# Kernel optimization log

Measured on AMD Instinct MI355X. Metric: run time of the kernel, lower is better.

## Reference

```python
import jax, jax.numpy as jnp
import numpy as np

B = 128            # trees per batch
D = 6              # complete binary tree depth
NPT = 2 ** (D + 1) - 1   # 127 nodes per tree
H = 450            # JTNN hidden size
V = 780            # junction-tree vocab size


def _build_forest():
    # complete binary trees; node 0 of each tree is the root
    child = np.arange(1, NPT)
    parent = (child - 1) // 2
    offs = (np.arange(B) * NPT)[:, None]
    ch = (child[None, :] + offs).ravel()
    pa = (parent[None, :] + offs).ravel()
    Eup = B * (NPT - 1)
    E = 2 * Eup
    # up (child->parent) edges first, then down (parent->child); +1 dummy pad row
    src = np.concatenate([ch, pa, [0]]).astype(np.int32)
    dst = np.concatenate([pa, ch, [0]]).astype(np.int32)
    rev = np.concatenate([np.arange(Eup) + Eup, np.arange(Eup), [E]]).astype(np.int32)
    depth_child = np.floor(np.log2(child + 1)).astype(np.int64)  # 1..D
    toff = np.arange(B)[:, None] * (NPT - 1)
    rows = []
    for d in range(D, 0, -1):        # bottom-up: deepest child level first
        t = np.nonzero(depth_child == d)[0]
        rows.append((t[None, :] + toff).ravel())
    for d in range(1, D + 1):        # top-down
        t = np.nonzero(depth_child == d)[0]
        rows.append((t[None, :] + toff).ravel() + Eup)
    Lmax = max(len(r) for r in rows)
    sched = np.full((len(rows), Lmax), E, dtype=np.int32)   # pad with dummy id E
    for i, r in enumerate(rows):
        sched[i, :len(r)] = r
    return src, dst, rev, sched


def setup_inputs() -> dict:
    key = jax.random.key(0)
    ks = jax.random.split(key, 8)
    src, dst, rev, sched = _build_forest()
    n_nodes = B * NPT
    p = lambda k, shp: jax.random.normal(k, shp, jnp.float32) * 0.05
    return {
        'wid': jax.random.randint(ks[0], (n_nodes,), 0, V).astype(jnp.int32),
        'src': jnp.asarray(src), 'dst': jnp.asarray(dst), 'rev': jnp.asarray(rev),
        'sched': jnp.asarray(sched),
        'emb': p(ks[1], (V, H)),
        'Wz': p(ks[2], (2 * H, H)), 'bz': jnp.zeros((H,), jnp.float32),
        'Wr': p(ks[3], (H, H)),
        'Ur': p(ks[4], (H, H)), 'bur': jnp.zeros((H,), jnp.float32),
        'Wh': p(ks[5], (2 * H, H)), 'bh': jnp.zeros((H,), jnp.float32),
        'Wg': p(ks[6], (2 * H, H)), 'bg': jnp.zeros((H,), jnp.float32),
    }


def _forward(wid, src, dst, rev, sched, emb, Wz, bz, Wr, Ur, bur, Wh, bh, Wg, bg):
    n_nodes = wid.shape[0]
    E = src.shape[0] - 1              # last slot is a dummy pad row
    x = emb[wid]                      # [N, H] node embeddings
    m = jnp.zeros((E + 1, x.shape[1]), x.dtype)   # edge messages (line-graph node state)
    rm = jnp.zeros_like(m)
    dstE = dst[:E]
    for lvl in range(sched.shape[0]):             # static number of tree levels
        eid = sched[lvl]                          # [Lmax], padded with E
        # pull: s/accum_rm = sum over predecessor line-graph nodes, i.e.
        # sum of m over in-edges of src[e] minus the backtracking (reverse) edge
        node_m = jax.ops.segment_sum(m[:E], dstE, num_segments=n_nodes)
        node_rm = jax.ops.segment_sum(rm[:E], dstE, num_segments=n_nodes)
        se, de = src[eid], dst[eid]
        s = node_m[se] - m[rev[eid]]
        arm = node_rm[se] - rm[rev[eid]]
        sx, dx = x[se], x[de]
        # GRUUpdate (DGL JTNN)
        z = jax.nn.sigmoid(jnp.concatenate([sx, s], 1) @ Wz + bz)
        mt = jnp.tanh(jnp.concatenate([sx, arm], 1) @ Wh + bh)
        m_new = (1.0 - z) * s + z * mt
        r = jax.nn.sigmoid(dx @ Wr + m_new @ Ur + bur)   # W_r has no bias
        m = m.at[eid].set(m_new)
        rm = rm.at[eid].set(r * m_new)
    # update_all: gather messages into destination nodes, then EncoderGatherUpdate
    node_m = jax.ops.segment_sum(m[:E], dstE, num_segments=n_nodes)
    h = jax.nn.relu(jnp.concatenate([x, node_m], 1) @ Wg + bg)   # [N, H]
    return h


def reference(wid, src, dst, rev, sched, emb, Wz, bz, Wr, Ur, bur, Wh, bh, Wg, bg):
    # returns h for all nodes; root_vecs = h[node_offsets] (roots are every NPT-th node)
    return _forward(wid, src, dst, rev, sched, emb, Wz, bz, Wr, Ur, bur, Wh, bh, Wg, bg)
```

## Files before the change

kernel.cpp:

```cpp
#include <hip/hip_runtime.h>
#include <math.h>

#define NTREES 128
#define NPT 127
#define NNODES (NTREES*NPT)
#define EUP (NTREES*(NPT-1))
#define HDIM 450
#define HP 512
#define LMAX 8192
#define NLVL 12

typedef unsigned short u16;
typedef __attribute__((ext_vector_type(8))) short bf16x8;
typedef __attribute__((ext_vector_type(4))) float f32x4;

__device__ __forceinline__ float sigmoidf_(float x) { return 1.f / (1.f + expf(-x)); }
__device__ __forceinline__ u16 f2b(float x) {
  unsigned u = __float_as_uint(x);
  return (u16)((u + 0x7FFFu + ((u >> 16) & 1u)) >> 16);
}
__device__ __forceinline__ float b2f(u16 h) { return __uint_as_float(((unsigned)h) << 16); }
__device__ __forceinline__ bf16x8 sub8(bf16x8 a, bf16x8 b) {
  bf16x8 r;
#pragma unroll
  for (int i = 0; i < 8; ++i) r[i] = (short)f2b(b2f((u16)a[i]) - b2f((u16)b[i]));
  return r;
}

__device__ __forceinline__ u16* ldsp(u16* base, int row, int slot) {
  return base + row * 64 + ((slot ^ (row & 7)) << 3);
}
#define MFMA(a, b, c) __builtin_amdgcn_mfma_f32_16x16x32_bf16(a, b, c, 0, 0, 0)

__global__ void zero_ws(float4* __restrict__ p, int n4) {
  int i = blockIdx.x * 256 + threadIdx.x;
  int stride = gridDim.x * 256;
  for (; i < n4; i += stride) p[i] = make_float4(0.f, 0.f, 0.f, 0.f);
}

__global__ void prep_pad(const float* __restrict__ Wz, const float* __restrict__ Wh,
                         const float* __restrict__ Wr, const float* __restrict__ Ur,
                         const float* __restrict__ Wg,
                         const float* __restrict__ bz, const float* __restrict__ bh,
                         const float* __restrict__ bur, const float* __restrict__ bg,
                         u16* __restrict__ WpreT, u16* __restrict__ WzbT,
                         u16* __restrict__ WhbT, u16* __restrict__ UrT,
                         u16* __restrict__ WgT, float* __restrict__ biasp) {
  int idx = blockIdx.x * 256 + threadIdx.x;
  if (idx < 1536 * 512) {
    int n = idx >> 9, k = idx & 511;
    int sel = n >> 9, j = n & 511;
    float v = 0.f;
    if (k < HDIM && j < HDIM) {
// ... 43 lines not shown
  int row = gid >> 6, g = gid & 63;
  int j0 = g * 8;
  const float* er = emb + (size_t)wid[row] * HDIM;
  float f[8] = {0.f, 0.f, 0.f, 0.f, 0.f, 0.f, 0.f, 0.f};
  if (j0 <= 440) {
#pragma unroll
    for (int q = 0; q < 4; ++q) {
      float2 p = *(const float2*)(er + j0 + q * 2);
      f[q * 2] = p.x; f[q * 2 + 1] = p.y;
    }
  } else if (j0 == 448) {
    f[0] = er[448]; f[1] = er[449];
  }
  bf16x8 v;
#pragma unroll
  for (int q = 0; q < 8; ++q) v[q] = (short)f2b(f[q]);
  *(bf16x8*)(xp + (size_t)row * HP + j0) = v;
}

__global__ __launch_bounds__(256, 4) void mfma_pre(
    const u16* __restrict__ xp, const u16* __restrict__ WpreT,
    u16* __restrict__ Xzh, u16* __restrict__ Xr) {
  __shared__ u16 Al[64 * 64], Bl[64 * 64];
  int tid = threadIdx.x;
  int n0 = blockIdx.x * 64, m0 = blockIdx.y * 64;
  int l = tid & 63, w = tid >> 6, wr = w >> 1, wc = w & 1, lr = l & 15, lq = l >> 4;
  int sr = tid >> 2, skc = tid & 3;
  const u16* abase = xp + (size_t)(m0 + sr) * HP + skc * 16;
  const u16* bbase = WpreT + (size_t)(n0 + sr) * HP + skc * 16;
  f32x4 acc[2][2] = {};
  for (int kt = 0; kt < HP; kt += 64) {
    *(bf16x8*)ldsp(Al, sr, 2 * skc) = ((const bf16x8*)(abase + kt))[0];
    *(bf16x8*)ldsp(Al, sr, 2 * skc + 1) = ((const bf16x8*)(abase + kt))[1];
    *(bf16x8*)ldsp(Bl, sr, 2 * skc) = ((const bf16x8*)(bbase + kt))[0];
    *(bf16x8*)ldsp(Bl, sr, 2 * skc + 1) = ((const bf16x8*)(bbase + kt))[1];
    __syncthreads();
#pragma unroll
    for (int kk = 0; kk < 64; kk += 32) {
      int slot = (kk >> 3) + lq;
      bf16x8 fa0 = *(bf16x8*)ldsp(Al, wr * 32 + lr, slot);
      bf16x8 fa1 = *(bf16x8*)ldsp(Al, wr * 32 + 16 + lr, slot);
      bf16x8 fb0 = *(bf16x8*)ldsp(Bl, wc * 32 + lr, slot);
      bf16x8 fb1 = *(bf16x8*)ldsp(Bl, wc * 32 + 16 + lr, slot);
      acc[0][0] = MFMA(fa0, fb0, acc[0][0]); acc[0][1] = MFMA(fa0, fb1, acc[0][1]);
      acc[1][0] = MFMA(fa1, fb0, acc[1][0]); acc[1][1] = MFMA(fa1, fb1, acc[1][1]);
    }
    __syncthreads();
  }
#pragma unroll
  for (int fi = 0; fi < 2; ++fi)
#pragma unroll
    for (int fj = 0; fj < 2; ++fj) {
      int colg = n0 + wc * 32 + fj * 16 + lr;
#pragma unroll
      for (int reg = 0; reg < 4; ++reg) {
        int row = m0 + wr * 32 + fi * 16 + lq * 4 + reg;
        u16 o = f2b(acc[fi][fj][reg]);
        if (colg < 1024) Xzh[(size_t)row * 1024 + colg] = o;
        else Xr[(size_t)row * HP + (colg - 1024)] = o;
      }
    }
}

__global__ void leaf_lvl0(const int* __restrict__ sched0, const int* __restrict__ src,
                          const u16* __restrict__ Xzh, const float* __restrict__ biasp,
                          u16* __restrict__ mup) {
  int gid = blockIdx.x * 256 + threadIdx.x;
  int r = gid >> 7, g = gid & 127;
  int e = sched0[r];
  int se = src[e];
  int col = g * 4;
  ushort4 xz = *(const ushort4*)(Xzh + (size_t)se * 1024 + col);
  ushort4 xh = *(const ushort4*)(Xzh + (size_t)se * 1024 + 512 + col);
  float4 bz = *(const float4*)(biasp + col);
  float4 bh = *(const float4*)(biasp + 512 + col);
  ushort4 o;
  o.x = f2b(sigmoidf_(b2f(xz.x) + bz.x) * tanhf(b2f(xh.x) + bh.x));
  o.y = f2b(sigmoidf_(b2f(xz.y) + bz.y) * tanhf(b2f(xh.y) + bh.y));
  o.z = f2b(sigmoidf_(b2f(xz.z) + bz.z) * tanhf(b2f(xh.z) + bh.z));
  o.w = f2b(sigmoidf_(b2f(xz.w) + bz.w) * tanhf(b2f(xh.w) + bh.w));
  *(ushort4*)(mup + (size_t)e * HP + col) = o;
}

__global__ __launch_bounds__(256, 4) void mfma_lvl1_up(
    const int* __restrict__ schedrow, const int* __restrict__ src,
    const u16* __restrict__ node_m, const u16* __restrict__ node_rm,
    const u16* __restrict__ Xzh, const u16* __restrict__ WzbT,
    const u16* __restrict__ WhbT, const float* __restrict__ biasp,
    u16* __restrict__ mup) {
  __shared__ u16 Asl[64 * 64], Aal[64 * 64], Bzl[64 * 64], Btl[64 * 64];
  __shared__ int e_s[64], se_s[64];
  int tid = threadIdx.x;
  int n0 = blockIdx.x * 64, m0 = blockIdx.y * 64;
  if (tid < 64) { int e = schedrow[m0 + tid]; e_s[tid] = e; se_s[tid] = src[e]; }
  __syncthreads();
  int l = tid & 63, w = tid >> 6, wr = w >> 1, wc = w & 1, lr = l & 15, lq = l >> 4;
  int sr = tid >> 2, skc = tid & 3;
  int se_st = se_s[sr];
  const u16* pmb = node_m + (size_t)se_st * HP + skc * 16;
  const u16* prb = node_rm + (size_t)se_st * HP + skc * 16;
  const u16* bzb = WzbT + (size_t)(n0 + sr) * HP + skc * 16;
  const u16* btb = WhbT + (size_t)(n0 + sr) * HP + skc * 16;
  f32x4 accZ[2][2] = {}, accT[2][2] = {};
  for (int kt = 0; kt < HP; kt += 64) {
    *(bf16x8*)ldsp(Asl, sr, 2 * skc) = ((const bf16x8*)(pmb + kt))[0];
    *(bf16x8*)ldsp(Asl, sr, 2 * skc + 1) = ((const bf16x8*)(pmb + kt))[1];
    *(bf16x8*)ldsp(Aal, sr, 2 * skc) = ((const bf16x8*)(prb + kt))[0];
    *(bf16x8*)ldsp(Aal, sr, 2 * skc + 1) = ((const bf16x8*)(prb + kt))[1];
    *(bf16x8*)ldsp(Bzl, sr, 2 * skc) = ((const bf16x8*)(bzb + kt))[0];
    *(bf16x8*)ldsp(Bzl, sr, 2 * skc + 1) = ((const bf16x8*)(bzb + kt))[1];
    *(bf16x8*)ldsp(Btl, sr, 2 * skc) = ((const bf16x8*)(btb + kt))[0];
    *(bf16x8*)ldsp(Btl, sr, 2 * skc + 1) = ((const bf16x8*)(btb + kt))[1];
    __syncthreads();
#pragma unroll
    for (int kk = 0; kk < 64; kk += 32) {
      int slot = (kk >> 3) + lq;
      bf16x8 a0 = *(bf16x8*)ldsp(Asl, wr * 32 + lr, slot);
      bf16x8 a1 = *(bf16x8*)ldsp(Asl, wr * 32 + 16 + lr, slot);
      bf16x8 c0 = *(bf16x8*)ldsp(Aal, wr * 32 + lr, slot);
      bf16x8 c1 = *(bf16x8*)ldsp(Aal, wr * 32 + 16 + lr, slot);
      bf16x8 z0 = *(bf16x8*)ldsp(Bzl, wc * 32 + lr, slot);
      bf16x8 z1 = *(bf16x8*)ldsp(Bzl, wc * 32 + 16 + lr, slot);
      bf16x8 t0 = *(bf16x8*)ldsp(Btl, wc * 32 + lr, slot);
      bf16x8 t1 = *(bf16x8*)ldsp(Btl, wc * 32 + 16 + lr, slot);
      accZ[0][0] = MFMA(a0, z0, accZ[0][0]); accZ[0][1] = MFMA(a0, z1, accZ[0][1]);
      accZ[1][0] = MFMA(a1, z0, accZ[1][0]); accZ[1][1] = MFMA(a1, z1, accZ[1][1]);
      accT[0][0] = MFMA(c0, t0, accT[0][0]); accT[0][1] = MFMA(c0, t1, accT[0][1]);
      accT[1][0] = MFMA(c1, t0, accT[1][0]); accT[1][1] = MFMA(c1, t1, accT[1][1]);
    }
    __syncthreads();
  }
#pragma unroll
  for (int fi = 0; fi < 2; ++fi)
#pragma unroll
    for (int fj = 0; fj < 2; ++fj) {
      int colg = n0 + wc * 32 + fj * 16 + lr;
#pragma unroll
      for (int reg = 0; reg < 4; ++reg) {
        int row = wr * 32 + fi * 16 + lq * 4 + reg;
        int e = e_s[row], se = se_s[row];
        float xz = b2f(Xzh[(size_t)se * 1024 + colg]);
        float xh = b2f(Xzh[(size_t)se * 1024 + 512 + colg]);
        float sv = b2f(node_m[(size_t)se * HP + colg]);
        float z = sigmoidf_(accZ[fi][fj][reg] + xz + biasp[colg]);
        float t = tanhf(accT[fi][fj][reg] + xh + biasp[512 + colg]);
        mup[(size_t)e * HP + colg] = f2b((1.f - z) * sv + z * t);
      }
    }
}

__global__ __launch_bounds__(256, 4) void mfma_lvl1_down(
    const int* __restrict__ schedrow, const int* __restrict__ src,
    const u16* __restrict__ node_m, const u16* __restrict__ node_rm,
    const u16* __restrict__ mup, const u16* __restrict__ rmup,
    const u16* __restrict__ Xzh, const u16* __restrict__ WzbT,
    const u16* __restrict__ WhbT, const float* __restrict__ biasp,
    u16* __restrict__ dtmp) {
  __shared__ u16 Asl[64 * 64], Aal[64 * 64], Bzl[64 * 64], Btl[64 * 64];
  __shared__ int se_s[64], eu_s[64];
  int tid = threadIdx.x;
  int n0 = blockIdx.x * 64, m0 = blockIdx.y * 64;
  if (tid < 64) { int e = schedrow[m0 + tid]; eu_s[tid] = e - EUP; se_s[tid] = src[e]; }
  __syncthreads();
  int l = tid & 63, w = tid >> 6, wr = w >> 1, wc = w & 1, lr = l & 15, lq = l >> 4;
  int sr = tid >> 2, skc = tid & 3;
  int se_st = se_s[sr], eu_st = eu_s[sr];
  const u16* pmb = node_m + (size_t)se_st * HP + skc * 16;
  const u16* pub = mup + (size_t)eu_st * HP + skc * 16;
  const u16* prb = node_rm + (size_t)se_st * HP + skc * 16;
  const u16* pvb = rmup + (size_t)eu_st * HP + skc * 16;
  const u16* bzb = WzbT + (size_t)(n0 + sr) * HP + skc * 16;
  const u16* btb = WhbT + (size_t)(n0 + sr) * HP + skc * 16;
  f32x4 accZ[2][2] = {}, accT[2][2] = {};
  for (int kt = 0; kt < HP; kt += 64) {
    *(bf16x8*)ldsp(Asl, sr, 2 * skc) = sub8(((const bf16x8*)(pmb + kt))[0], ((const bf16x8*)(pub + kt))[0]);
    *(bf16x8*)ldsp(Asl, sr, 2 * skc + 1) = sub8(((const bf16x8*)(pmb + kt))[1], ((const bf16x8*)(pub + kt))[1]);
    *(bf16x8*)ldsp(Aal, sr, 2 * skc) = sub8(((const bf16x8*)(prb + kt))[0], ((const bf16x8*)(pvb + kt))[0]);
    *(bf16x8*)ldsp(Aal, sr, 2 * skc + 1) = sub8(((const bf16x8*)(prb + kt))[1], ((const bf16x8*)(pvb + kt))[1]);
    *(bf16x8*)ldsp(Bzl, sr, 2 * skc) = ((const bf16x8*)(bzb + kt))[0];
    *(bf16x8*)ldsp(Bzl, sr, 2 * skc + 1) = ((const bf16x8*)(bzb + kt))[1];
    *(bf16x8*)ldsp(Btl, sr, 2 * skc) = ((const bf16x8*)(btb + kt))[0];
    *(bf16x8*)ldsp(Btl, sr, 2 * skc + 1) = ((const bf16x8*)(btb + kt))[1];
    __syncthreads();
#pragma unroll
    for (int kk = 0; kk < 64; kk += 32) {
      int slot = (kk >> 3) + lq;
      bf16x8 a0 = *(bf16x8*)ldsp(Asl, wr * 32 + lr, slot);
      bf16x8 a1 = *(bf16x8*)ldsp(Asl, wr * 32 + 16 + lr, slot);
      bf16x8 c0 = *(bf16x8*)ldsp(Aal, wr * 32 + lr, slot);
      bf16x8 c1 = *(bf16x8*)ldsp(Aal, wr * 32 + 16 + lr, slot);
      bf16x8 z0 = *(bf16x8*)ldsp(Bzl, wc * 32 + lr, slot);
      bf16x8 z1 = *(bf16x8*)ldsp(Bzl, wc * 32 + 16 + lr, slot);
      bf16x8 t0 = *(bf16x8*)ldsp(Btl, wc * 32 + lr, slot);
      bf16x8 t1 = *(bf16x8*)ldsp(Btl, wc * 32 + 16 + lr, slot);
      accZ[0][0] = MFMA(a0, z0, accZ[0][0]); accZ[0][1] = MFMA(a0, z1, accZ[0][1]);
      accZ[1][0] = MFMA(a1, z0, accZ[1][0]); accZ[1][1] = MFMA(a1, z1, accZ[1][1]);
      accT[0][0] = MFMA(c0, t0, accT[0][0]); accT[0][1] = MFMA(c0, t1, accT[0][1]);
      accT[1][0] = MFMA(c1, t0, accT[1][0]); accT[1][1] = MFMA(c1, t1, accT[1][1]);
    }
    __syncthreads();
  }
#pragma unroll
  for (int fi = 0; fi < 2; ++fi)
#pragma unroll
    for (int fj = 0; fj < 2; ++fj) {
      int colg = n0 + wc * 32 + fj * 16 + lr;
#pragma unroll
      for (int reg = 0; reg < 4; ++reg) {
        int row = wr * 32 + fi * 16 + lq * 4 + reg;
        int se = se_s[row], eu = eu_s[row];
        float xz = b2f(Xzh[(size_t)se * 1024 + colg]);
        float xh = b2f(Xzh[(size_t)se * 1024 + 512 + colg]);
        float sv = b2f(node_m[(size_t)se * HP + colg]) - b2f(mup[(size_t)eu * HP + colg]);
        float z = sigmoidf_(accZ[fi][fj][reg] + xz + biasp[colg]);
        float t = tanhf(accT[fi][fj][reg] + xh + biasp[512 + colg]);
        dtmp[(size_t)(m0 + row) * HP + colg] = f2b((1.f - z) * sv + z * t);
      }
    }
}

__global__ __launch_bounds__(256, 4) void mfma_lvl2_up(
    const int* __restrict__ schedrow, const int* __restrict__ dst,
    const u16* __restrict__ mup, u16* __restrict__ rmup,
    u16* __restrict__ node_m, u16* __restrict__ node_rm,
    const u16* __restrict__ Xr, const u16* __restrict__ UrT,
    const float* __restrict__ biasp) {
  __shared__ u16 Al[64 * 64], Bl[64 * 64];
  __shared__ int e_s[64], de_s[64];
  int tid = threadIdx.x;
  int n0 = blockIdx.x * 64, m0 = blockIdx.y * 64;
  if (tid < 64) { int e = schedrow[m0 + tid]; e_s[tid] = e; de_s[tid] = dst[e]; }
  __syncthreads();
  int l = tid & 63, w = tid >> 6, wr = w >> 1, wc = w & 1, lr = l & 15, lq = l >> 4;
  int sr = tid >> 2, skc = tid & 3;
  const u16* ab = mup + (size_t)e_s[sr] * HP + skc * 16;
  const u16* bb = UrT + (size_t)(n0 + sr) * HP + skc * 16;
  f32x4 acc[2][2] = {};
  for (int kt = 0; kt < HP; kt += 64) {
    *(bf16x8*)ldsp(Al, sr, 2 * skc) = ((const bf16x8*)(ab + kt))[0];
    *(bf16x8*)ldsp(Al, sr, 2 * skc + 1) = ((const bf16x8*)(ab + kt))[1];
    *(bf16x8*)ldsp(Bl, sr, 2 * skc) = ((const bf16x8*)(bb + kt))[0];
    *(bf16x8*)ldsp(Bl, sr, 2 * skc + 1) = ((const bf16x8*)(bb + kt))[1];
    __syncthreads();
#pragma unroll
    for (int kk = 0; kk < 64; kk += 32) {
      int slot = (kk >> 3) + lq;
      bf16x8 fa0 = *(bf16x8*)ldsp(Al, wr * 32 + lr, slot);
      bf16x8 fa1 = *(bf16x8*)ldsp(Al, wr * 32 + 16 + lr, slot);
      bf16x8 fb0 = *(bf16x8*)ldsp(Bl, wc * 32 + lr, slot);
      bf16x8 fb1 = *(bf16x8*)ldsp(Bl, wc * 32 + 16 + lr, slot);
      acc[0][0] = MFMA(fa0, fb0, acc[0][0]); acc[0][1] = MFMA(fa0, fb1, acc[0][1]);
      acc[1][0] = MFMA(fa1, fb0, acc[1][0]); acc[1][1] = MFMA(fa1, fb1, acc[1][1]);
    }
    __syncthreads();
  }
#pragma unroll
  for (int fi = 0; fi < 2; ++fi)
#pragma unroll
    for (int fj = 0; fj < 2; ++fj) {
      int colg = n0 + wc * 32 + fj * 16 + lr;
      int rowbase = wr * 32 + fi * 16 + lq * 4;
      float mv[4], rmv[4];
#pragma unroll
      for (int reg = 0; reg < 4; ++reg) {
        int row = rowbase + reg;
        int e = e_s[row], de = de_s[row];
        mv[reg] = b2f(mup[(size_t)e * HP + colg]);
        float r = sigmoidf_(acc[fi][fj][reg] + b2f(Xr[(size_t)de * HP + colg]) + biasp[1024 + colg]);
        rmv[reg] = r * mv[reg];
        rmup[(size_t)e * HP + colg] = f2b(rmv[reg]);
      }
      int de0 = de_s[rowbase], de2 = de_s[rowbase + 2];
      node_m[(size_t)de0 * HP + colg] = f2b(mv[0] + mv[1]);
      node_rm[(size_t)de0 * HP + colg] = f2b(rmv[0] + rmv[1]);
      node_m[(size_t)de2 * HP + colg] = f2b(mv[2] + mv[3]);
      node_rm[(size_t)de2 * HP + colg] = f2b(rmv[2] + rmv[3]);
    }
}

__global__ __launch_bounds__(256, 4) void mfma_lvl2_down(
    const int* __restrict__ schedrow, const int* __restrict__ dst,
    const u16* __restrict__ dtmp,
    u16* __restrict__ node_m, u16* __restrict__ node_rm,
    const u16* __restrict__ Xr, const u16* __restrict__ UrT,
    const float* __restrict__ biasp) {
  __shared__ u16 Al[64 * 64], Bl[64 * 64];
  __shared__ int de_s[64];
  int tid = threadIdx.x;
  int n0 = blockIdx.x * 64, m0 = blockIdx.y * 64;
  if (tid < 64) de_s[tid] = dst[schedrow[m0 + tid]];
  __syncthreads();
  int l = tid & 63, w = tid >> 6, wr = w >> 1, wc = w & 1, lr = l & 15, lq = l >> 4;
  int sr = tid >> 2, skc = tid & 3;
  const u16* ab = dtmp + (size_t)(m0 + sr) * HP + skc * 16;
  const u16* bb = UrT + (size_t)(n0 + sr) * HP + skc * 16;
  f32x4 acc[2][2] = {};
  for (int kt = 0; kt < HP; kt += 64) {
    *(bf16x8*)ldsp(Al, sr, 2 * skc) = ((const bf16x8*)(ab + kt))[0];
    *(bf16x8*)ldsp(Al, sr, 2 * skc + 1) = ((const bf16x8*)(ab + kt))[1];
    *(bf16x8*)ldsp(Bl, sr, 2 * skc) = ((const bf16x8*)(bb + kt))[0];
    *(bf16x8*)ldsp(Bl, sr, 2 * skc + 1) = ((const bf16x8*)(bb + kt))[1];
    __syncthreads();
#pragma unroll
    for (int kk = 0; kk < 64; kk += 32) {
      int slot = (kk >> 3) + lq;
      bf16x8 fa0 = *(bf16x8*)ldsp(Al, wr * 32 + lr, slot);
      bf16x8 fa1 = *(bf16x8*)ldsp(Al, wr * 32 + 16 + lr, slot);
      bf16x8 fb0 = *(bf16x8*)ldsp(Bl, wc * 32 + lr, slot);
      bf16x8 fb1 = *(bf16x8*)ldsp(Bl, wc * 32 + 16 + lr, slot);
      acc[0][0] = MFMA(fa0, fb0, acc[0][0]); acc[0][1] = MFMA(fa0, fb1, acc[0][1]);
      acc[1][0] = MFMA(fa1, fb0, acc[1][0]); acc[1][1] = MFMA(fa1, fb1, acc[1][1]);
    }
    __syncthreads();
  }
#pragma unroll
  for (int fi = 0; fi < 2; ++fi)
#pragma unroll
    for (int fj = 0; fj < 2; ++fj) {
      int colg = n0 + wc * 32 + fj * 16 + lr;
#pragma unroll
      for (int reg = 0; reg < 4; ++reg) {
        int row = wr * 32 + fi * 16 + lq * 4 + reg;
        int de = de_s[row];
        size_t nidx = (size_t)de * HP + colg;
        float mv = b2f(dtmp[(size_t)(m0 + row) * HP + colg]);
        float r = sigmoidf_(acc[fi][fj][reg] + b2f(Xr[nidx]) + biasp[1024 + colg]);
        node_m[nidx] = f2b(b2f(node_m[nidx]) + mv);
        node_rm[nidx] = f2b(b2f(node_rm[nidx]) + r * mv);
      }
    }
}

__global__ __launch_bounds__(256, 4) void mfma_final(
    const u16* __restrict__ xp, const u16* __restrict__ node_m,
    const u16* __restrict__ WgT, const float* __restrict__ biasp,
    float* __restrict__ out) {
  __shared__ u16 Al[64 * 64], Bl[64 * 64];
  int tid = threadIdx.x;
  int n0 = blockIdx.x * 64, m0 = blockIdx.y * 64;
  int l = tid & 63, w = tid >> 6, wr = w >> 1, wc = w & 1, lr = l & 15, lq = l >> 4;
  int sr = tid >> 2, skc = tid & 3;
  const u16* axb = xp + (size_t)(m0 + sr) * HP + skc * 16;
  const u16* anb = node_m + (size_t)(m0 + sr) * HP + skc * 16;
  const u16* bb = WgT + (size_t)(n0 + sr) * 1024 + skc * 16;
  f32x4 acc[2][2] = {};
  for (int kt = 0; kt < 1024; kt += 64) {
    const u16* ap = (kt < HP) ? (axb + kt) : (anb + (kt - HP));
    *(bf16x8*)ldsp(Al, sr, 2 * skc) = ((const bf16x8*)ap)[0];
    *(bf16x8*)ldsp(Al, sr, 2 * skc + 1) = ((const bf16x8*)ap)[1];
    *(bf16x8*)ldsp(Bl, sr, 2 * skc) = ((const bf16x8*)(bb + kt))[0];
    *(bf16x8*)ldsp(Bl, sr, 2 * skc + 1) = ((const bf16x8*)(bb + kt))[1];
    __syncthreads();
#pragma unroll
    for (int kk = 0; kk < 64; kk += 32) {
      int slot = (kk >> 3) + lq;
      bf16x8 fa0 = *(bf16x8*)ldsp(Al, wr * 32 + lr, slot);
      bf16x8 fa1 = *(bf16x8*)ldsp(Al, wr * 32 + 16 + lr, slot);
      bf16x8 fb0 = *(bf16x8*)ldsp(Bl, wc * 32 + lr, slot);
      bf16x8 fb1 = *(bf16x8*)ldsp(Bl, wc * 32 + 16 + lr, slot);
      acc[0][0] = MFMA(fa0, fb0, acc[0][0]); acc[0][1] = MFMA(fa0, fb1, acc[0][1]);
      acc[1][0] = MFMA(fa1, fb0, acc[1][0]); acc[1][1] = MFMA(fa1, fb1, acc[1][1]);
    }
// ... 22 lines not shown
  const int* dst = (const int*)d_in[2];
  const int* sched = (const int*)d_in[4];
  const float* emb = (const float*)d_in[5];
  const float* Wz = (const float*)d_in[6];
  const float* bz = (const float*)d_in[7];
  const float* Wr = (const float*)d_in[8];
  const float* Ur = (const float*)d_in[9];
  const float* bur = (const float*)d_in[10];
  const float* Wh = (const float*)d_in[11];
  const float* bh = (const float*)d_in[12];
  const float* Wg = (const float*)d_in[13];
  const float* bg = (const float*)d_in[14];
  float* out = (float*)d_out;
  float* ws = (float*)d_ws;

  size_t o = 0;
  u16* x_p = (u16*)(ws + o);     o += (size_t)NNODES * HP / 2;
  u16* Xzh = (u16*)(ws + o);     o += (size_t)NNODES * 1024 / 2;
  u16* Xr = (u16*)(ws + o);      o += (size_t)NNODES * HP / 2;
  u16* node_m = (u16*)(ws + o);  o += (size_t)NNODES * HP / 2;
  u16* node_rm = (u16*)(ws + o); o += (size_t)NNODES * HP / 2;
  u16* mup = (u16*)(ws + o);     o += (size_t)EUP * HP / 2;
  u16* rmup = (u16*)(ws + o);    o += (size_t)EUP * HP / 2;
  u16* dtmp = (u16*)(ws + o);    o += (size_t)LMAX * HP / 2;
  u16* WpreT = (u16*)(ws + o);   o += (size_t)1536 * HP / 2;
  u16* WzbT = (u16*)(ws + o);    o += (size_t)HP * HP / 2;
  u16* WhbT = (u16*)(ws + o);    o += (size_t)HP * HP / 2;
  u16* UrT = (u16*)(ws + o);     o += (size_t)HP * HP / 2;
  u16* WgT = (u16*)(ws + o);     o += (size_t)HP * 1024 / 2;
  float* biasp = ws + o;         o += (size_t)4 * HP;
  if (ws_size < o * sizeof(float)) return;

  size_t zbytes = (size_t)2 * NNODES * HP * 2;
  zero_ws<<<2048, 256, 0, stream>>>((float4*)node_m, (int)(zbytes / 16));

  int prep_elems = 1536 * 512 + 3 * 262144 + 512 * 1024 + 4 * HP;
  prep_pad<<<(prep_elems + 255) / 256, 256, 0, stream>>>(
      Wz, Wh, Wr, Ur, Wg, bz, bh, bur, bg, WpreT, WzbT, WhbT, UrT, WgT, biasp);

  gather_embed<<<(NNODES * 64 + 255) / 256, 256, 0, stream>>>(wid, emb, x_p);

  mfma_pre<<<dim3(1536 / 64, NNODES / 64), 256, 0, stream>>>(x_p, WpreT, Xzh, Xr);

  for (int lvl = 0; lvl < NLVL; ++lvl) {
    int L = (lvl < 6) ? (LMAX >> lvl) : (256 << (lvl - 6));
    const int* schedrow = sched + (size_t)lvl * LMAX;
    if (lvl == 0) {
      leaf_lvl0<<<4096, 256, 0, stream>>>(schedrow, src, Xzh, biasp, mup);
    } else if (lvl < 6) {
      mfma_lvl1_up<<<dim3(8, L / 64), 256, 0, stream>>>(
          schedrow, src, node_m, node_rm, Xzh, WzbT, WhbT, biasp, mup);
    } else {
      mfma_lvl1_down<<<dim3(8, L / 64), 256, 0, stream>>>(
          schedrow, src, node_m, node_rm, mup, rmup, Xzh, WzbT, WhbT, biasp, dtmp);
    }
    if (lvl < 6) {
      mfma_lvl2_up<<<dim3(8, L / 64), 256, 0, stream>>>(
          schedrow, dst, mup, rmup, node_m, node_rm, Xr, UrT, biasp);
    } else {
      mfma_lvl2_down<<<dim3(8, L / 64), 256, 0, stream>>>(
          schedrow, dst, dtmp, node_m, node_rm, Xr, UrT, biasp);
    }
  }

  mfma_final<<<dim3(8, NNODES / 64), 256, 0, stream>>>(x_p, node_m, WgT, biasp, out);
}
```

Measured before the change: 624.1 us.

## Fuse per-level GRU gate and reset GEMMs into one kernel per level

Replaces the two kernels per tree level (gate/candidate GEMM and reset GEMM) with a single fused_level kernel. Each block owns 32 edges across the full hidden width and keeps the A rows and the new messages in shared memory, so the intermediate dtmp buffer and the extra mup round trips go away. The leaf level is also folded in. In addition, mfma_pre and mfma_final use a 1D grid remapped so that row tiles are spread across XCDs for L2 locality. The trade-off is that each block now recomputes the full N range serially with 32-row tiles, which lowers parallelism and occupancy (launch bounds 2) on the small upper levels.

```diff
diff --git a/kernel.cpp b/kernel.cpp
--- a/kernel.cpp
+++ b/kernel.cpp
@@ -29,6 +29,9 @@
 
 __device__ __forceinline__ u16* ldsp(u16* base, int row, int slot) {
   return base + row * 64 + ((slot ^ (row & 7)) << 3);
+}
+__device__ __forceinline__ int physA(int row, int lslot) {
+  return row * 512 + (((lslot & ~7) | ((lslot & 7) ^ (row & 7))) << 3);
 }
 #define MFMA(a, b, c) __builtin_amdgcn_mfma_f32_16x16x32_bf16(a, b, c, 0, 0, 0)
 
@@ -118,8 +121,13 @@
     const u16* __restrict__ xp, const u16* __restrict__ WpreT,
     u16* __restrict__ Xzh, u16* __restrict__ Xr) {
   __shared__ u16 Al[64 * 64], Bl[64 * 64];
+  int bid = blockIdx.x;
+  int xcd = bid & 7, q0 = bid >> 3;
+  int nt = q0 % 24;
+  int mt = (q0 / 24) * 8 + xcd;
+  if (mt >= NNODES / 64) return;
+  int n0 = nt * 64, m0 = mt * 64;
   int tid = threadIdx.x;
-  int n0 = blockIdx.x * 64, m0 = blockIdx.y * 64;
   int l = tid & 63, w = tid >> 6, wr = w >> 1, wc = w & 1, lr = l & 15, lq = l >> 4;
   int sr = tid >> 2, skc = tid & 3;
   const u16* abase = xp + (size_t)(m0 + sr) * HP + skc * 16;
@@ -158,273 +166,228 @@
     }
 }
 
-__global__ void leaf_lvl0(const int* __restrict__ sched0, const int* __restrict__ src,
-                          const u16* __restrict__ Xzh, const float* __restrict__ biasp,
-                          u16* __restrict__ mup) {
-  int gid = blockIdx.x * 256 + threadIdx.x;
-  int r = gid >> 7, g = gid & 127;
-  int e = sched0[r];
-  int se = src[e];
-  int col = g * 4;
-  ushort4 xz = *(const ushort4*)(Xzh + (size_t)se * 1024 + col);
-  ushort4 xh = *(const ushort4*)(Xzh + (size_t)se * 1024 + 512 + col);
-  float4 bz = *(const float4*)(biasp + col);
-  float4 bh = *(const float4*)(biasp + 512 + col);
-  ushort4 o;
-  o.x = f2b(sigmoidf_(b2f(xz.x) + bz.x) * tanhf(b2f(xh.x) + bh.x));
-  o.y = f2b(sigmoidf_(b2f(xz.y) + bz.y) * tanhf(b2f(xh.y) + bh.y));
-  o.z = f2b(sigmoidf_(b2f(xz.z) + bz.z) * tanhf(b2f(xh.z) + bh.z));
-  o.w = f2b(sigmoidf_(b2f(xz.w) + bz.w) * tanhf(b2f(xh.w) + bh.w));
-  *(ushort4*)(mup + (size_t)e * HP + col) = o;
-}
-
-__global__ __launch_bounds__(256, 4) void mfma_lvl1_up(
-    const int* __restrict__ schedrow, const int* __restrict__ src,
-    const u16* __restrict__ node_m, const u16* __restrict__ node_rm,
-    const u16* __restrict__ Xzh, const u16* __restrict__ WzbT,
-    const u16* __restrict__ WhbT, const float* __restrict__ biasp,
-    u16* __restrict__ mup) {
-  __shared__ u16 Asl[64 * 64], Aal[64 * 64], Bzl[64 * 64], Btl[64 * 64];
-  __shared__ int e_s[64], se_s[64];
+__global__ __launch_bounds__(256, 2) void fused_level(
+    int mode, const int* __restrict__ schedrow, const int* __restrict__ src,
+    const int* __restrict__ dst,
+    u16* __restrict__ node_m, u16* __restrict__ node_rm,
+    u16* __restrict__ mup, u16* __restrict__ rmup,
+    const u16* __restrict__ Xzh, const u16* __restrict__ Xr,
+    const u16* __restrict__ WzbT, const u16* __restrict__ WhbT,
+    const u16* __restrict__ UrT, const float* __restrict__ biasp) {
+  __shared__ __align__(16) u16 As[32 * 512];
+  __shared__ __align__(16) u16 Aa[32 * 512];
+  __shared__ __align__(16) u16 Bz[64 * 64];
+  __shared__ __align__(16) u16 Bt[64 * 64];
   int tid = threadIdx.x;
-  int n0 = blockIdx.x * 64, m0 = blockIdx.y * 64;
-  if (tid < 64) { int e = schedrow[m0 + tid]; e_s[tid] = e; se_s[tid] = src[e]; }
+  int m0 = blockIdx.x * 32;
+
+  int srow = tid >> 3, sj = tid & 7;
+  int e_st = schedrow[m0 + srow];
+  int se_st = src[e_st];
+  if (mode == 0) {
+    const u16* pm = node_m + (size_t)se_st * HP;
+    const u16* pr = node_rm + (size_t)se_st * HP;
+#pragma unroll
+    for (int q = 0; q < 8; ++q) {
+      int ls = (sj ^ (srow & 7)) + q * 8;
+      int col = ls * 8;
+      *(bf16x8*)&As[physA(srow, ls)] = *(const bf16x8*)(pm + col);
+      *(bf16x8*)&Aa[physA(srow, ls)] = *(const bf16x8*)(pr + col);
+    }
+  } else if (mode == 1) {
+    int eu = e_st - EUP;
+    const u16* pm = node_m + (size_t)se_st * HP;
+    const u16* pu = mup + (size_t)eu * HP;
+    const u16* pr = node_rm + (size_t)se_st * HP;
+    const u16* pv = rmup + (size_t)eu * HP;
+#pragma unroll
+    for (int q = 0; q < 8; ++q) {
+      int ls = (sj ^ (srow & 7)) + q * 8;
+      int col = ls * 8;
+      *(bf16x8*)&As[physA(srow, ls)] =
+          sub8(*(const bf16x8*)(pm + col), *(const bf16x8*)(pu + col));
+      *(bf16x8*)&Aa[physA(srow, ls)] =
+          sub8(*(const bf16x8*)(pr + col), *(const bf16x8*)(pv + col));
+    }
+  } else {
+    const u16* xzp = Xzh + (size_t)se_st * 1024;
+    u16* mo = mup + (size_t)e_st * HP;
+#pragma unroll
+    for (int q = 0; q < 8; ++q) {
+      int ls = (sj ^ (srow & 7)) + q * 8;
+      int col = ls * 8;
+      bf16x8 vz = *(const bf16x8*)(xzp + col);
+      bf16x8 vh = *(const bf16x8*)(xzp + 512 + col);
+      bf16x8 o;
+#pragma unroll
+      for (int k = 0; k < 8; ++k) {
+        float z = sigmoidf_(b2f((u16)vz[k]) + biasp[col + k]);
+        float t = tanhf(b2f((u16)vh[k]) + biasp[512 + col + k]);
+        o[k] = (short)f2b(z * t);
+      }
+      *(bf16x8*)&As[physA(srow, ls)] = o;
+      *(bf16x8*)(mo + col) = o;
+    }
+  }
   __syncthreads();
-  int l = tid & 63, w = tid >> 6, wr = w >> 1, wc = w & 1, lr = l & 15, lq = l >> 4;
-  int sr = tid >> 2, skc = tid & 3;
-  int se_st = se_s[sr];
-  const u16* pmb = node_m + (size_t)se_st * HP + skc * 16;
-  const u16* prb = node_rm + (size_t)se_st * HP + skc * 16;
-  const u16* bzb = WzbT + (size_t)(n0 + sr) * HP + skc * 16;
-  const u16* btb = WhbT + (size_t)(n0 + sr) * HP + skc * 16;
-  f32x4 accZ[2][2] = {}, accT[2][2] = {};
-  for (int kt = 0; kt < HP; kt += 64) {
-    *(bf16x8*)ldsp(Asl, sr, 2 * skc) = ((const bf16x8*)(pmb + kt))[0];
-    *(bf16x8*)ldsp(Asl, sr, 2 * skc + 1) = ((const bf16x8*)(pmb + kt))[1];
-    *(bf16x8*)ldsp(Aal, sr, 2 * skc) = ((const bf16x8*)(prb + kt))[0];
-    *(bf16x8*)ldsp(Aal, sr, 2 * skc + 1) = ((const bf16x8*)(prb + kt))[1];
-    *(bf16x8*)ldsp(Bzl, sr, 2 * skc) = ((const bf16x8*)(bzb + kt))[0];
-    *(bf16x8*)ldsp(Bzl, sr, 2 * skc + 1) = ((const bf16x8*)(bzb + kt))[1];
-    *(bf16x8*)ldsp(Btl, sr, 2 * skc) = ((const bf16x8*)(btb + kt))[0];
-    *(bf16x8*)ldsp(Btl, sr, 2 * skc + 1) = ((const bf16x8*)(btb + kt))[1];
+
+  int l = tid & 63, w = tid >> 6;
+  int wr = w >> 1, wc = w & 1, lr = l & 15, lq = l >> 4;
+  int bsr = tid >> 2, bskc = tid & 3;
+  int rowb = wr * 16 + lq * 4;
+  int e_r[4], se_r[4], de_r[4];
+#pragma unroll
+  for (int i = 0; i < 4; ++i) {
+    e_r[i] = schedrow[m0 + rowb + i];
+    se_r[i] = src[e_r[i]];
+    de_r[i] = dst[e_r[i]];
+  }
+
+  float mn[8][8];
+  if (mode < 2) {
+#pragma unroll
+    for (int t8 = 0; t8 < 8; ++t8) {
+      f32x4 aZ[2] = {}, aT[2] = {};
+      for (int kt8 = 0; kt8 < 8; ++kt8) {
+        const u16* bz = WzbT + (size_t)(t8 * 64 + bsr) * HP + kt8 * 64 + bskc * 16;
+        const u16* bt = WhbT + (size_t)(t8 * 64 + bsr) * HP + kt8 * 64 + bskc * 16;
+        *(bf16x8*)ldsp(Bz, bsr, 2 * bskc) = ((const bf16x8*)bz)[0];
+        *(bf16x8*)ldsp(Bz, bsr, 2 * bskc + 1) = ((const bf16x8*)bz)[1];
+        *(bf16x8*)ldsp(Bt, bsr, 2 * bskc) = ((const bf16x8*)bt)[0];
+        *(bf16x8*)ldsp(Bt, bsr, 2 * bskc + 1) = ((const bf16x8*)bt)[1];
+        __syncthreads();
+#pragma unroll
+        for (int kk = 0; kk < 2; ++kk) {
+          int arow = wr * 16 + lr;
+          bf16x8 a0 = *(const bf16x8*)&As[physA(arow, kt8 * 8 + kk * 4 + lq)];
+          bf16x8 c0 = *(const bf16x8*)&Aa[physA(arow, kt8 * 8 + kk * 4 + lq)];
+          bf16x8 z0 = *(const bf16x8*)ldsp(Bz, wc * 32 + lr, kk * 4 + lq);
+          bf16x8 z1 = *(const bf16x8*)ldsp(Bz, wc * 32 + 16 + lr, kk * 4 + lq);
+          bf16x8 t0 = *(const bf16x8*)ldsp(Bt, wc * 32 + lr, kk * 4 + lq);
+          bf16x8 t1 = *(const bf16x8*)ldsp(Bt, wc * 32 + 16 + lr, kk * 4 + lq);
+          aZ[0] = MFMA(a0, z0, aZ[0]); aZ[1] = MFMA(a0, z1, aZ[1]);
+          aT[0] = MFMA(c0, t0, aT[0]); aT[1] = MFMA(c0, t1, aT[1]);
+        }
+        __syncthreads();
+      }
+#pragma unroll
+      for (int fj = 0; fj < 2; ++fj)
+#pragma unroll
+        for (int reg = 0; reg < 4; ++reg) {
+          int row = rowb + reg;
+          int lcol = t8 * 64 + wc * 32 + fj * 16 + lr;
+          float s = b2f(As[physA(row, lcol >> 3) + (lcol & 7)]);
+          float xz = b2f(Xzh[(size_t)se_r[reg] * 1024 + lcol]);
+          float xh = b2f(Xzh[(size_t)se_r[reg] * 1024 + 512 + lcol]);
+          float z = sigmoidf_(aZ[fj][reg] + xz + biasp[lcol]);
+          float t = tanhf(aT[fj][reg] + xh + biasp[512 + lcol]);
+          mn[t8][fj * 4 + reg] = (1.f - z) * s + z * t;
+        }
+    }
     __syncthreads();
 #pragma unroll
-    for (int kk = 0; kk < 64; kk += 32) {
-      int slot = (kk >> 3) + lq;
-      bf16x8 a0 = *(bf16x8*)ldsp(Asl, wr * 32 + lr, slot);
-      bf16x8 a1 = *(bf16x8*)ldsp(Asl, wr * 32 + 16 + lr, slot);
-      bf16x8 c0 = *(bf16x8*)ldsp(Aal, wr * 32 + lr, slot);
-      bf16x8 c1 = *(bf16x8*)ldsp(Aal, wr * 32 + 16 + lr, slot);
-      bf16x8 z0 = *(bf16x8*)ldsp(Bzl, wc * 32 + lr, slot);
-      bf16x8 z1 = *(bf16x8*)ldsp(Bzl, wc * 32 + 16 + lr, slot);
-      bf16x8 t0 = *(bf16x8*)ldsp(Btl, wc * 32 + lr, slot);
-      bf16x8 t1 = *(bf16x8*)ldsp(Btl, wc * 32 + 16 + lr, slot);
-      accZ[0][0] = MFMA(a0, z0, accZ[0][0]); accZ[0][1] = MFMA(a0, z1, accZ[0][1]);
-      accZ[1][0] = MFMA(a1, z0, accZ[1][0]); accZ[1][1] = MFMA(a1, z1, accZ[1][1]);
-      accT[0][0] = MFMA(c0, t0, accT[0][0]); accT[0][1] = MFMA(c0, t1, accT[0][1]);
-      accT[1][0] = MFMA(c1, t0, accT[1][0]); accT[1][1] = MFMA(c1, t1, accT[1][1]);
-    }
+    for (int t8 = 0; t8 < 8; ++t8)
+#pragma unroll
+      for (int fj = 0; fj < 2; ++fj)
+#pragma unroll
+        for (int reg = 0; reg < 4; ++reg) {
+          int row = rowb + reg;
+          int lcol = t8 * 64 + wc * 32 + fj * 16 + lr;
+          As[physA(row, lcol >> 3) + (lcol & 7)] = f2b(mn[t8][fj * 4 + reg]);
+        }
     __syncthreads();
-  }
-#pragma unroll
-  for (int fi = 0; fi < 2; ++fi)
-#pragma unroll
-    for (int fj = 0; fj < 2; ++fj) {
-      int colg = n0 + wc * 32 + fj * 16 + lr;
+    if (mode == 0) {
+      u16* mo = mup + (size_t)e_st * HP;
+#pragma unroll
+      for (int q = 0; q < 8; ++q) {
+        int ls = (sj ^ (srow & 7)) + q * 8;
+        *(bf16x8*)(mo + ls * 8) = *(const bf16x8*)&As[physA(srow, ls)];
+      }
+    }
+  }
+
+#pragma unroll
+  for (int t8 = 0; t8 < 8; ++t8) {
+    f32x4 aR[2] = {};
+    for (int kt8 = 0; kt8 < 8; ++kt8) {
+      const u16* bu = UrT + (size_t)(t8 * 64 + bsr) * HP + kt8 * 64 + bskc * 16;
+      *(bf16x8*)ldsp(Bz, bsr, 2 * bskc) = ((const bf16x8*)bu)[0];
+      *(bf16x8*)ldsp(Bz, bsr, 2 * bskc + 1) = ((const bf16x8*)bu)[1];
+      __syncthreads();
+#pragma unroll
+      for (int kk = 0; kk < 2; ++kk) {
+        int arow = wr * 16 + lr;
+        bf16x8 a0 = *(const bf16x8*)&As[physA(arow, kt8 * 8 + kk * 4 + lq)];
+        bf16x8 b0 = *(const bf16x8*)ldsp(Bz, wc * 32 + lr, kk * 4 + lq);
+        bf16x8 b1 = *(const bf16x8*)ldsp(Bz, wc * 32 + 16 + lr, kk * 4 + lq);
+        aR[0] = MFMA(a0, b0, aR[0]); aR[1] = MFMA(a0, b1, aR[1]);
+      }
+      __syncthreads();
+    }
+#pragma unroll
+    for (int fj = 0; fj < 2; ++fj)
 #pragma unroll
       for (int reg = 0; reg < 4; ++reg) {
-        int row = wr * 32 + fi * 16 + lq * 4 + reg;
-        int e = e_s[row], se = se_s[row];
-        float xz = b2f(Xzh[(size_t)se * 1024 + colg]);
-        float xh = b2f(Xzh[(size_t)se * 1024 + 512 + colg]);
-        float sv = b2f(node_m[(size_t)se * HP + colg]);
-        float z = sigmoidf_(accZ[fi][fj][reg] + xz + biasp[colg]);
-        float t = tanhf(accT[fi][fj][reg] + xh + biasp[512 + colg]);
-        mup[(size_t)e * HP + colg] = f2b((1.f - z) * sv + z * t);
-      }
-    }
-}
-
-__global__ __launch_bounds__(256, 4) void mfma_lvl1_down(
-    const int* __restrict__ schedrow, const int* __restrict__ src,
-    const u16* __restrict__ node_m, const u16* __restrict__ node_rm,
-    const u16* __restrict__ mup, const u16* __restrict__ rmup,
-    const u16* __restrict__ Xzh, const u16* __restrict__ WzbT,
-    const u16* __restrict__ WhbT, const float* __restrict__ biasp,
-    u16* __restrict__ dtmp) {
-  __shared__ u16 Asl[64 * 64], Aal[64 * 64], Bzl[64 * 64], Btl[64 * 64];
-  __shared__ int se_s[64], eu_s[64];
-  int tid = threadIdx.x;
-  int n0 = blockIdx.x * 64, m0 = blockIdx.y * 64;
-  if (tid < 64) { int e = schedrow[m0 + tid]; eu_s[tid] = e - EUP; se_s[tid] = src[e]; }
+        int row = rowb + reg;
+        int lcol = t8 * 64 + wc * 32 + fj * 16 + lr;
+        float r = sigmoidf_(aR[fj][reg] + b2f(Xr[(size_t)de_r[reg] * HP + lcol]) +
+                            biasp[1024 + lcol]);
+        float mv = b2f(As[physA(row, lcol >> 3) + (lcol & 7)]);
+        Aa[physA(row, lcol >> 3) + (lcol & 7)] = f2b(r * mv);
+      }
+  }
   __syncthreads();
-  int l = tid & 63, w = tid >> 6, wr = w >> 1, wc = w & 1, lr = l & 15, lq = l >> 4;
-  int sr = tid >> 2, skc = tid & 3;
-  int se_st = se_s[sr], eu_st = eu_s[sr];
-  const u16* pmb = node_m + (size_t)se_st * HP + skc * 16;
-  const u16* pub = mup + (size_t)eu_st * HP + skc * 16;
-  const u16* prb = node_rm + (size_t)se_st * HP + skc * 16;
-  const u16* pvb = rmup + (size_t)eu_st * HP + skc * 16;
-  const u16* bzb = WzbT + (size_t)(n0 + sr) * HP + skc * 16;
-  const u16* btb = WhbT + (size_t)(n0 + sr) * HP + skc * 16;
-  f32x4 accZ[2][2] = {}, accT[2][2] = {};
-  for (int kt = 0; kt < HP; kt += 64) {
-    *(bf16x8*)ldsp(Asl, sr, 2 * skc) = sub8(((const bf16x8*)(pmb + kt))[0], ((const bf16x8*)(pub + kt))[0]);
-    *(bf16x8*)ldsp(Asl, sr, 2 * skc + 1) = sub8(((const bf16x8*)(pmb + kt))[1], ((const bf16x8*)(pub + kt))[1]);
-    *(bf16x8*)ldsp(Aal, sr, 2 * skc) = sub8(((const bf16x8*)(prb + kt))[0], ((const bf16x8*)(pvb + kt))[0]);
-    *(bf16x8*)ldsp(Aal, sr, 2 * skc + 1) = sub8(((const bf16x8*)(prb + kt))[1], ((const bf16x8*)(pvb + kt))[1]);
-    *(bf16x8*)ldsp(Bzl, sr, 2 * skc) = ((const bf16x8*)(bzb + kt))[0];
-    *(bf16x8*)ldsp(Bzl, sr, 2 * skc + 1) = ((const bf16x8*)(bzb + kt))[1];
-    *(bf16x8*)ldsp(Btl, sr, 2 * skc) = ((const bf16x8*)(btb + kt))[0];
-    *(bf16x8*)ldsp(Btl, sr, 2 * skc + 1) = ((const bf16x8*)(btb + kt))[1];
-    __syncthreads();
-#pragma unroll
-    for (int kk = 0; kk < 64; kk += 32) {
-      int slot = (kk >> 3) + lq;
-      bf16x8 a0 = *(bf16x8*)ldsp(Asl, wr * 32 + lr, slot);
-      bf16x8 a1 = *(bf16x8*)ldsp(Asl, wr * 32 + 16 + lr, slot);
-      bf16x8 c0 = *(bf16x8*)ldsp(Aal, wr * 32 + lr, slot);
-      bf16x8 c1 = *(bf16x8*)ldsp(Aal, wr * 32 + 16 + lr, slot);
-      bf16x8 z0 = *(bf16x8*)ldsp(Bzl, wc * 32 + lr, slot);
-      bf16x8 z1 = *(bf16x8*)ldsp(Bzl, wc * 32 + 16 + lr, slot);
-      bf16x8 t0 = *(bf16x8*)ldsp(Btl, wc * 32 + lr, slot);
-      bf16x8 t1 = *(bf16x8*)ldsp(Btl, wc * 32 + 16 + lr, slot);
-      accZ[0][0] = MFMA(a0, z0, accZ[0][0]); accZ[0][1] = MFMA(a0, z1, accZ[0][1]);
-      accZ[1][0] = MFMA(a1, z0, accZ[1][0]); accZ[1][1] = MFMA(a1, z1, accZ[1][1]);
-      accT[0][0] = MFMA(c0, t0, accT[0][0]); accT[0][1] = MFMA(c0, t1, accT[0][1]);
-      accT[1][0] = MFMA(c1, t0, accT[1][0]); accT[1][1] = MFMA(c1, t1, accT[1][1]);
-    }
-    __syncthreads();
-  }
-#pragma unroll
-  for (int fi = 0; fi < 2; ++fi)
-#pragma unroll
-    for (int fj = 0; fj < 2; ++fj) {
-      int colg = n0 + wc * 32 + fj * 16 + lr;
-#pragma unroll
-      for (int reg = 0; reg < 4; ++reg) {
-        int row = wr * 32 + fi * 16 + lq * 4 + reg;
-        int se = se_s[row], eu = eu_s[row];
-        float xz = b2f(Xzh[(size_t)se * 1024 + colg]);
-        float xh = b2f(Xzh[(size_t)se * 1024 + 512 + colg]);
-        float sv = b2f(node_m[(size_t)se * HP + colg]) - b2f(mup[(size_t)eu * HP + colg]);
-        float z = sigmoidf_(accZ[fi][fj][reg] + xz + biasp[colg]);
-        float t = tanhf(accT[fi][fj][reg] + xh + biasp[512 + colg]);
-        dtmp[(size_t)(m0 + row) * HP + colg] = f2b((1.f - z) * sv + z * t);
-      }
-    }
-}
-
-__global__ __launch_bounds__(256, 4) void mfma_lvl2_up(
-    const int* __restrict__ schedrow, const int* __restrict__ dst,
-    const u16* __restrict__ mup, u16* __restrict__ rmup,
-    u16* __restrict__ node_m, u16* __restrict__ node_rm,
-    const u16* __restrict__ Xr, const u16* __restrict__ UrT,
-    const float* __restrict__ biasp) {
-  __shared__ u16 Al[64 * 64], Bl[64 * 64];
-  __shared__ int e_s[64], de_s[64];
-  int tid = threadIdx.x;
-  int n0 = blockIdx.x * 64, m0 = blockIdx.y * 64;
-  if (tid < 64) { int e = schedrow[m0 + tid]; e_s[tid] = e; de_s[tid] = dst[e]; }
-  __syncthreads();
-  int l = tid & 63, w = tid >> 6, wr = w >> 1, wc = w & 1, lr = l & 15, lq = l >> 4;
-  int sr = tid >> 2, skc = tid & 3;
-  const u16* ab = mup + (size_t)e_s[sr] * HP + skc * 16;
-  const u16* bb = UrT + (size_t)(n0 + sr) * HP + skc * 16;
-  f32x4 acc[2][2] = {};
-  for (int kt = 0; kt < HP; kt += 64) {
-    *(bf16x8*)ldsp(Al, sr, 2 * skc) = ((const bf16x8*)(ab + kt))[0];
-    *(bf16x8*)ldsp(Al, sr, 2 * skc + 1) = ((const bf16x8*)(ab + kt))[1];
-    *(bf16x8*)ldsp(Bl, sr, 2 * skc) = ((const bf16x8*)(bb + kt))[0];
-    *(bf16x8*)ldsp(Bl, sr, 2 * skc + 1) = ((const bf16x8*)(bb + kt))[1];
-    __syncthreads();
-#pragma unroll
-    for (int kk = 0; kk < 64; kk += 32) {
-      int slot = (kk >> 3) + lq;
-      bf16x8 fa0 = *(bf16x8*)ldsp(Al, wr * 32 + lr, slot);
-      bf16x8 fa1 = *(bf16x8*)ldsp(Al, wr * 32 + 16 + lr, slot);
-      bf16x8 fb0 = *(bf16x8*)ldsp(Bl, wc * 32 + lr, slot);
-      bf16x8 fb1 = *(bf16x8*)ldsp(Bl, wc * 32 + 16 + lr, slot);
-      acc[0][0] = MFMA(fa0, fb0, acc[0][0]); acc[0][1] = MFMA(fa0, fb1, acc[0][1]);
-      acc[1][0] = MFMA(fa1, fb0, acc[1][0]); acc[1][1] = MFMA(fa1, fb1, acc[1][1]);
-    }
-    __syncthreads();
-  }
-#pragma unroll
-  for (int fi = 0; fi < 2; ++fi)
-#pragma unroll
-    for (int fj = 0; fj < 2; ++fj) {
-      int colg = n0 + wc * 32 + fj * 16 + lr;
-      int rowbase = wr * 32 + fi * 16 + lq * 4;
-      float mv[4], rmv[4];
-#pragma unroll
-      for (int reg = 0; reg < 4; ++reg) {
-        int row = rowbase + reg;
-        int e = e_s[row], de = de_s[row];
-        mv[reg] = b2f(mup[(size_t)e * HP + colg]);
-        float r = sigmoidf_(acc[fi][fj][reg] + b2f(Xr[(size_t)de * HP + colg]) + biasp[1024 + colg]);
-        rmv[reg] = r * mv[reg];
-        rmup[(size_t)e * HP + colg] = f2b(rmv[reg]);
-      }
-      int de0 = de_s[rowbase], de2 = de_s[rowbase + 2];
-      node_m[(size_t)de0 * HP + colg] = f2b(mv[0] + mv[1]);
-      node_rm[(size_t)de0 * HP + colg] = f2b(rmv[0] + rmv[1]);
-      node_m[(size_t)de2 * HP + colg] = f2b(mv[2] + mv[3]);
-      node_rm[(size_t)de2 * HP + colg] = f2b(rmv[2] + rmv[3]);
-    }
-}
-
-__global__ __launch_bounds__(256, 4) void mfma_lvl2_down(
-    const int* __restrict__ schedrow, const int* __restrict__ dst,
-    const u16* __restrict__ dtmp,
-    u16* __restrict__ node_m, u16* __restrict__ node_rm,
-    const u16* __restrict__ Xr, const u16* __restrict__ UrT,
-    const float* __restrict__ biasp) {
-  __shared__ u16 Al[64 * 64], Bl[64 * 64];
-  __shared__ int de_s[64];
-  int tid = threadIdx.x;
-  int n0 = blockIdx.x * 64, m0 = blockIdx.y * 64;
-  if (tid < 64) de_s[tid] = dst[schedrow[m0 + tid]];
-  __syncthreads();
-  int l = tid & 63, w = tid >> 6, wr = w >> 1, wc = w & 1, lr = l & 15, lq = l >> 4;
-  int sr = tid >> 2, skc = tid & 3;
-  const u16* ab = dtmp + (size_t)(m0 + sr) * HP + skc * 16;
-  const u16* bb = UrT + (size_t)(n0 + sr) * HP + skc * 16;
-  f32x4 acc[2][2] = {};
-  for (int kt = 0; kt < HP; kt += 64) {
-    *(bf16x8*)ldsp(Al, sr, 2 * skc) = ((const bf16x8*)(ab + kt))[0];
-    *(bf16x8*)ldsp(Al, sr, 2 * skc + 1) = ((const bf16x8*)(ab + kt))[1];
-    *(bf16x8*)ldsp(Bl, sr, 2 * skc) = ((const bf16x8*)(bb + kt))[0];
-    *(bf16x8*)ldsp(Bl, sr, 2 * skc + 1) = ((const bf16x8*)(bb + kt))[1];
-    __syncthreads();
-#pragma unroll
-    for (int kk = 0; kk < 64; kk += 32) {
-      int slot = (kk >> 3) + lq;
-      bf16x8 fa0 = *(bf16x8*)ldsp(Al, wr * 32 + lr, slot);
-      bf16x8 fa1 = *(bf16x8*)ldsp(Al, wr * 32 + 16 + lr, slot);
-      bf16x8 fb0 = *(bf16x8*)ldsp(Bl, wc * 32 + lr, slot);
-      bf16x8 fb1 = *(bf16x8*)ldsp(Bl, wc * 32 + 16 + lr, slot);
-      acc[0][0] = MFMA(fa0, fb0, acc[0][0]); acc[0][1] = MFMA(fa0, fb1, acc[0][1]);
-      acc[1][0] = MFMA(fa1, fb0, acc[1][0]); acc[1][1] = MFMA(fa1, fb1, acc[1][1]);
-    }
-    __syncthreads();
-  }
-#pragma unroll
-  for (int fi = 0; fi < 2; ++fi)
-#pragma unroll
-    for (int fj = 0; fj < 2; ++fj) {
-      int colg = n0 + wc * 32 + fj * 16 + lr;
-#pragma unroll
-      for (int reg = 0; reg < 4; ++reg) {
-        int row = wr * 32 + fi * 16 + lq * 4 + reg;
-        int de = de_s[row];
-        size_t nidx = (size_t)de * HP + colg;
-        float mv = b2f(dtmp[(size_t)(m0 + row) * HP + colg]);
-        float r = sigmoidf_(acc[fi][fj][reg] + b2f(Xr[nidx]) + biasp[1024 + colg]);
-        node_m[nidx] = f2b(b2f(node_m[nidx]) + mv);
-        node_rm[nidx] = f2b(b2f(node_rm[nidx]) + r * mv);
-      }
-    }
+
+  if (mode == 1) {
+    int de = dst[e_st];
+    u16* nm = node_m + (size_t)de * HP;
+    u16* nr = node_rm + (size_t)de * HP;
+#pragma unroll
+    for (int q = 0; q < 8; ++q) {
+      int ls = (sj ^ (srow & 7)) + q * 8;
+      int col = ls * 8;
+      bf16x8 mv = *(const bf16x8*)&As[physA(srow, ls)];
+      bf16x8 rv = *(const bf16x8*)&Aa[physA(srow, ls)];
+      bf16x8 om = *(const bf16x8*)(nm + col);
+      bf16x8 orr = *(const bf16x8*)(nr + col);
+      bf16x8 sm, sr2;
+#pragma unroll
+      for (int k = 0; k < 8; ++k) {
+        sm[k] = (short)f2b(b2f((u16)om[k]) + b2f((u16)mv[k]));
+        sr2[k] = (short)f2b(b2f((u16)orr[k]) + b2f((u16)rv[k]));
+      }
+      *(bf16x8*)(nm + col) = sm;
+      *(bf16x8*)(nr + col) = sr2;
+    }
+  } else {
+    u16* ro = rmup + (size_t)e_st * HP;
+#pragma unroll
+    for (int q = 0; q < 8; ++q) {
+      int ls = (sj ^ (srow & 7)) + q * 8;
+      *(bf16x8*)(ro + ls * 8) = *(const bf16x8*)&Aa[physA(srow, ls)];
+    }
+    int p = tid >> 4, l16 = tid & 15;
+    int dep = dst[schedrow[m0 + 2 * p]];
+    u16* nm = node_m + (size_t)dep * HP;
+    u16* nr = node_rm + (size_t)dep * HP;
+#pragma unroll
+    for (int q = 0; q < 4; ++q) {
+      int ls = l16 + q * 16;
+      int col = ls * 8;
+      bf16x8 a0 = *(const bf16x8*)&As[physA(2 * p, ls)];
+      bf16x8 a1 = *(const bf16x8*)&As[physA(2 * p + 1, ls)];
+      bf16x8 r0 = *(const bf16x8*)&Aa[physA(2 * p, ls)];
+      bf16x8 r1 = *(const bf16x8*)&Aa[physA(2 * p + 1, ls)];
+      bf16x8 sm, sr2;
+#pragma unroll
+      for (int k = 0; k < 8; ++k) {
+        sm[k] = (short)f2b(b2f((u16)a0[k]) + b2f((u16)a1[k]));
+        sr2[k] = (short)f2b(b2f((u16)r0[k]) + b2f((u16)r1[k]));
+      }
+      *(bf16x8*)(nm + col) = sm;
+      *(bf16x8*)(nr + col) = sr2;
+    }
+  }
 }
 
 __global__ __launch_bounds__(256, 4) void mfma_final(
@@ -432,8 +395,13 @@
     const u16* __restrict__ WgT, const float* __restrict__ biasp,
     float* __restrict__ out) {
   __shared__ u16 Al[64 * 64], Bl[64 * 64];
+  int bid = blockIdx.x;
+  int xcd = bid & 7, q0 = bid >> 3;
+  int nt = q0 % 8;
+  int mt = (q0 / 8) * 8 + xcd;
+  if (mt >= NNODES / 64) return;
+  int n0 = nt * 64, m0 = mt * 64;
   int tid = threadIdx.x;
-  int n0 = blockIdx.x * 64, m0 = blockIdx.y * 64;
   int l = tid & 63, w = tid >> 6, wr = w >> 1, wc = w & 1, lr = l & 15, lq = l >> 4;
   int sr = tid >> 2, skc = tid & 3;
   const u16* axb = xp + (size_t)(m0 + sr) * HP + skc * 16;
@@ -502,7 +470,6 @@
   u16* node_rm = (u16*)(ws + o); o += (size_t)NNODES * HP / 2;
   u16* mup = (u16*)(ws + o);     o += (size_t)EUP * HP / 2;
   u16* rmup = (u16*)(ws + o);    o += (size_t)EUP * HP / 2;
-  u16* dtmp = (u16*)(ws + o);    o += (size_t)LMAX * HP / 2;
   u16* WpreT = (u16*)(ws + o);   o += (size_t)1536 * HP / 2;
   u16* WzbT = (u16*)(ws + o);    o += (size_t)HP * HP / 2;
   u16* WhbT = (u16*)(ws + o);    o += (size_t)HP * HP / 2;
@@ -520,28 +487,16 @@
 
   gather_embed<<<(NNODES * 64 + 255) / 256, 256, 0, stream>>>(wid, emb, x_p);
 
-  mfma_pre<<<dim3(1536 / 64, NNODES / 64), 256, 0, stream>>>(x_p, WpreT, Xzh, Xr);
+  mfma_pre<<<256 * 24, 256, 0, stream>>>(x_p, WpreT, Xzh, Xr);
 
   for (int lvl = 0; lvl < NLVL; ++lvl) {
     int L = (lvl < 6) ? (LMAX >> lvl) : (256 << (lvl - 6));
     const int* schedrow = sched + (size_t)lvl * LMAX;
-    if (lvl == 0) {
-      leaf_lvl0<<<4096, 256, 0, stream>>>(schedrow, src, Xzh, biasp, mup);
-    } else if (lvl < 6) {
-      mfma_lvl1_up<<<dim3(8, L / 64), 256, 0, stream>>>(
-          schedrow, src, node_m, node_rm, Xzh, WzbT, WhbT, biasp, mup);
-    } else {
-      mfma_lvl1_down<<<dim3(8, L / 64), 256, 0, stream>>>(
-          schedrow, src, node_m, node_rm, mup, rmup, Xzh, WzbT, WhbT, biasp, dtmp);
-    }
-    if (lvl < 6) {
-      mfma_lvl2_up<<<dim3(8, L / 64), 256, 0, stream>>>(
-          schedrow, dst, mup, rmup, node_m, node_rm, Xr, UrT, biasp);
-    } else {
-      mfma_lvl2_down<<<dim3(8, L / 64), 256, 0, stream>>>(
-          schedrow, dst, dtmp, node_m, node_rm, Xr, UrT, biasp);
-    }
-  }
-
-  mfma_final<<<dim3(8, NNODES / 64), 256, 0, stream>>>(x_p, node_m, WgT, biasp, out);
-}
+    int mode = (lvl == 0) ? 2 : (lvl < 6 ? 0 : 1);
+    fused_level<<<L / 32, 256, 0, stream>>>(
+        mode, schedrow, src, dst, node_m, node_rm, mup, rmup,
+        Xzh, Xr, WzbT, WhbT, UrT, biasp);
+  }
+
+  mfma_final<<<256 * 8, 256, 0, stream>>>(x_p, node_m, WgT, biasp, out);
+}
```

Result: slower. 1.858 ms (+197.7%).
